# Kernel optimization log

Hardware: AMD Instinct MI355X
Metric: run time of the kernel (lower is better)

The kernel has to match this reference:

```python
import jax, jax.numpy as jnp
import numpy as np

CROSSOVER_MAGNITUDE = 0.3
MUTATION_FACTOR = 0.3

B, A, H = 16, 512, 8  # batch, activation_size (== dim_emb), n_head


def setup_inputs() -> dict:
    key = jax.random.key(0)
    ks = jax.random.split(key, 11)
    d = A
    s = 0.02  # small init scale for weights
    return {
        "Q": jax.random.normal(ks[0], (B, A, A), jnp.float32),
        "K": jax.random.normal(ks[1], (B, A, A), jnp.float32),
        "V": jax.random.normal(ks[2], (B, A), jnp.float32),
        "WQ_w": jax.random.normal(ks[3], (d, d), jnp.float32) * s,
        "WQ_b": jax.random.normal(ks[4], (d,), jnp.float32) * s,
        "WK_w": jax.random.normal(ks[5], (d, d), jnp.float32) * s,
        "WK_b": jax.random.normal(ks[6], (d,), jnp.float32) * s,
        "WV_w": jax.random.normal(ks[7], (d, d), jnp.float32) * s,
        "WV_b": jax.random.normal(ks[8], (d,), jnp.float32) * s,
        "WO_w": jax.random.normal(ks[9], (d, d * H), jnp.float32) * s,
        "WO_b": jax.random.normal(ks[10], (d,), jnp.float32) * s,
    }


def _attention_core(Qp, Kp, Vp, WO_w, WO_b):
    # Qp, Kp: (B, A, A) projected; identical across heads in the original
    # (heads are copies stacked before shared Linear), so compute once
    # and broadcast. Vp: (B, A).
    rkey = jax.random.key(42)
    kp, km, kr1, kr2 = jax.random.split(rkey, 4)

    am0 = jnp.einsum('bji,bjk->bik', Qp, Kp) / jnp.sqrt(jnp.float32(8.0))
    am = jnp.broadcast_to(am0[:, None], (B, H, A, A))  # (B,H,A,A)

    def mutate(a):
        # elementwise multiply by U(1-mf, 1+mf) noise
        m = jax.random.uniform(km, a.shape, jnp.float32,
                               1.0 - MUTATION_FACTOR, 1.0 + MUTATION_FACTOR)
        return a * m

    def crossover(a):
        # swap the tail segments [c:] of two random rows per (batch, head)
        c = A - int(A * CROSSOVER_MAGNITUDE)
        r1 = jax.random.randint(kr1, (B, H), 0, A)
        r2 = jax.random.randint(kr2, (B, H), 0, A)
        bi = jnp.arange(B)[:, None]
        hi = jnp.arange(H)[None, :]
        tails = a[..., c:]                     # (B,H,A,A-c)
        t1 = tails[bi, hi, r1]                 # (B,H,A-c)
        t2 = tails[bi, hi, r2]
        tails = tails.at[bi, hi, r1].set(t2).at[bi, hi, r2].set(t1)
        return jnp.concatenate([a[..., :c], tails], axis=-1)

    p = jax.random.uniform(kp, ())
    am = jax.lax.cond(p <= 0.6, mutate, crossover, am)

    attn = jax.nn.softmax(am, axis=-1)               # (B,H,A,A)
    out = jnp.einsum('bhij,bj->bhi', attn, Vp)       # attn @ V[...,None] squeezed
    out = out.reshape(B, H * A)
    return out @ WO_w.T + WO_b                       # (B, A)


def reference(Q, K, V, WQ_w, WQ_b, WK_w, WK_b, WV_w, WV_b, WO_w, WO_b):
    Qp = Q @ WQ_w.T + WQ_b   # (B,A,A), same for every head
    Kp = K @ WK_w.T + WK_b
    Vp = V @ WV_w.T + WV_b   # (B,A)
    return _attention_core(Qp, Kp, Vp, WO_w, WO_b)
```

## Files before the change

### kernel.cpp

```cpp
#include <hip/hip_runtime.h>
#include <stdint.h>
#include <string.h>

#define B_ 16
#define A_ 512
#define H_ 8
#define C_CROSS 359
#define LDSTRIDE 40

typedef short short8 __attribute__((ext_vector_type(8)));
typedef float floatx4 __attribute__((ext_vector_type(4)));

__host__ __device__ __forceinline__ uint32_t rotl32(uint32_t x, int r) {
#ifdef __HIP_DEVICE_COMPILE__
  return __builtin_amdgcn_alignbit(x, x, 32 - r);
#else
  return (x << r) | (x >> (32 - r));
#endif
}

__host__ __device__ __forceinline__ void tf2x32(uint32_t k0, uint32_t k1,
                                                uint32_t x0, uint32_t x1,
                                                uint32_t& o0, uint32_t& o1) {
  uint32_t ks2 = k0 ^ k1 ^ 0x1BD11BDAu;
  x0 += k0; x1 += k1;
#define TFR(r) { x0 += x1; x1 = rotl32(x1, r); x1 ^= x0; }
  TFR(13) TFR(15) TFR(26) TFR(6)   x0 += k1;  x1 += ks2 + 1u;
  TFR(17) TFR(29) TFR(16) TFR(24)  x0 += ks2; x1 += k0 + 2u;
  TFR(13) TFR(15) TFR(26) TFR(6)   x0 += k0;  x1 += k1 + 3u;
  TFR(17) TFR(29) TFR(16) TFR(24)  x0 += k1;  x1 += ks2 + 4u;
  TFR(13) TFR(15) TFR(26) TFR(6)   x0 += ks2; x1 += k0 + 5u;
#undef TFR
  o0 = x0; o1 = x1;
}

__host__ __device__ __forceinline__ float bits2u01(uint32_t bits) {
  uint32_t v = (bits >> 9) | 0x3f800000u;
  float f;
#ifdef __HIP_DEVICE_COMPILE__
  f = __uint_as_float(v);
#else
  memcpy(&f, &v, 4);
#endif
  return f - 1.0f;
}

__device__ __forceinline__ float exp2_native(float x) {
  float r;
  asm("v_exp_f32 %0, %1\n\ts_nop 0" : "=v"(r) : "v"(x));
  return r;
}

__device__ __forceinline__ void tsplit(float x, short& h, short& l) {
  uint32_t u = __float_as_uint(x);
  float hf = __uint_as_float(u & 0xffff0000u);
  h = (short)(u >> 16);
  l = (short)(__float_as_uint(x - hf) >> 16);
}

__device__ __forceinline__ void tsplit8(const float4& v0, const float4& v1,
                                        short8& h, short8& l) {
  float xs[8] = {v0.x, v0.y, v0.z, v0.w, v1.x, v1.y, v1.z, v1.w};
#pragma unroll
  for (int j = 0; j < 8; ++j) {
    short hh, ll;
    tsplit(xs[j], hh, ll);
    h[j] = hh; l[j] = ll;
  }
}

__global__ __launch_bounds__(256, 2) void lin_mfma2(
    const float* __restrict__ Xq, const float* __restrict__ Wq,
    const float* __restrict__ bq, ushort* __restrict__ QptH, ushort* __restrict__ QptL,
    const float* __restrict__ Xk, const float* __restrict__ Wk,
    const float* __restrict__ bk, ushort* __restrict__ KptH, ushort* __restrict__ KptL) {
  int bid = blockIdx.x;
  int z = bid >> 8;
  int rem = bid & 255;
  int ti = rem >> 2, tn = rem & 3;
  const float* X = z ? Xk : Xq;
  const float* W = z ? Wk : Wq;
  const float* bias = z ? bk : bq;
  ushort* OH = z ? KptH : QptH;
  ushort* OL = z ? KptL : QptL;

  __shared__ __align__(16) char smem[40960];
  ushort (*Ah)[LDSTRIDE] = (ushort(*)[LDSTRIDE])(smem);
  ushort (*Al)[LDSTRIDE] = (ushort(*)[LDSTRIDE])(smem + 10240);
  ushort (*Bh)[LDSTRIDE] = (ushort(*)[LDSTRIDE])(smem + 20480);
  ushort (*Bl)[LDSTRIDE] = (ushort(*)[LDSTRIDE])(smem + 30720);
  uint32_t (*cs)[132] = (uint32_t(*)[132])(smem);

  int tid = threadIdx.x;
  int w = tid >> 6, lane = tid & 63, quad = lane >> 4, l16 = lane & 15;
  int wm = (w >> 1) * 64, wn = (w & 1) * 64;
  int m0 = ti * 128;
  int n0 = tn * 128;

  float bv[4];
#pragma unroll
  for (int nt = 0; nt < 4; ++nt) bv[nt] = bias[n0 + wn + nt * 16 + l16];

  const float* pX[2];
  const float* pW[2];
  int mW[2], kgW[2];
#pragma unroll
  for (int g = 0; g < 2; ++g) {
    int gid = g * 256 + tid;
    int m = gid >> 2, kg = gid & 3;
    mW[g] = m; kgW[g] = kg;
    pX[g] = X + (size_t)(m0 + m) * 512 + kg * 8;
    pW[g] = W + (size_t)(n0 + m) * 512 + kg * 8;
  }

  float4 ra[2][2], rb[2][2];
#pragma unroll
  for (int g = 0; g < 2; ++g) {
    ra[g][0] = *(const float4*)(pX[g]);
    ra[g][1] = *(const float4*)(pX[g] + 4);
    rb[g][0] = *(const float4*)(pW[g]);
    rb[g][1] = *(const float4*)(pW[g] + 4);
  }

  floatx4 acc[4][4] = {};

  for (int k0 = 0; k0 < 512; k0 += 32) {
    __syncthreads();
#pragma unroll
    for (int g = 0; g < 2; ++g) {
      short8 h8, l8;
      tsplit8(ra[g][0], ra[g][1], h8, l8);
      *(short8*)&Ah[mW[g]][kgW[g] * 8] = h8;
      *(short8*)&Al[mW[g]][kgW[g] * 8] = l8;
      tsplit8(rb[g][0], rb[g][1], h8, l8);
      *(short8*)&Bh[mW[g]][kgW[g] * 8] = h8;
      *(short8*)&Bl[mW[g]][kgW[g] * 8] = l8;
    }
    __syncthreads();
    if (k0 < 480) {
      int kn = k0 + 32;
#pragma unroll
      for (int g = 0; g < 2; ++g) {
        ra[g][0] = *(const float4*)(pX[g] + kn);
        ra[g][1] = *(const float4*)(pX[g] + kn + 4);
        rb[g][0] = *(const float4*)(pW[g] + kn);
        rb[g][1] = *(const float4*)(pW[g] + kn + 4);
      }
    }
    short8 fAh[4], fAl[4], fBh[4], fBl[4];
#pragma unroll
    for (int t4 = 0; t4 < 4; ++t4) {
      int ma = wm + t4 * 16 + l16;
      int nb = wn + t4 * 16 + l16;
      fAh[t4] = *(const short8*)&Ah[ma][quad * 8];
      fAl[t4] = *(const short8*)&Al[ma][quad * 8];
      fBh[t4] = *(const short8*)&Bh[nb][quad * 8];
      fBl[t4] = *(const short8*)&Bl[nb][quad * 8];
    }
#pragma unroll
    for (int mt = 0; mt < 4; ++mt)
#pragma unroll
      for (int nt = 0; nt < 4; ++nt) {
        acc[mt][nt] = __builtin_amdgcn_mfma_f32_16x16x32_bf16(fAh[mt], fBh[nt], acc[mt][nt], 0, 0, 0);
        acc[mt][nt] = __builtin_amdgcn_mfma_f32_16x16x32_bf16(fAh[mt], fBl[nt], acc[mt][nt], 0, 0, 0);
        acc[mt][nt] = __builtin_amdgcn_mfma_f32_16x16x32_bf16(fAl[mt], fBh[nt], acc[mt][nt], 0, 0, 0);
      }
  }

  __syncthreads();
  int bb = m0 >> 9, i0 = m0 & 511;
  for (int p = 0; p < 2; ++p) {
    if ((w & 1) == p) {
#pragma unroll
      for (int mt = 0; mt < 4; ++mt)
#pragma unroll
        for (int nt = 0; nt < 4; ++nt)
#pragma unroll
          for (int rr = 0; rr < 4; ++rr) {
            float val = acc[mt][nt][rr] + bv[nt];
            uint32_t u = __float_as_uint(val);
            uint32_t hi = u & 0xffff0000u;
            uint32_t lo = __float_as_uint(val - __uint_as_float(hi)) >> 16;
            cs[nt * 16 + l16][wm + mt * 16 + quad * 4 + rr] = hi | lo;
          }
    }
    __syncthreads();
    {
      int col_l = tid >> 2, iseg = (tid & 3) * 32;
      int d = n0 + p * 64 + col_l;
      size_t obase = ((size_t)(bb * 512 + d)) * 512 + i0 + iseg;
      ushort* oh = OH + obase;
      ushort* ol = OL + obase;
#pragma unroll
      for (int sgi = 0; sgi < 4; ++sgi) {
        short8 hv, lv;
#pragma unroll
        for (int j = 0; j < 8; ++j) {
          uint32_t v = cs[col_l][iseg + sgi * 8 + j];
          hv[j] = (short)(v >> 16);
          lv[j] = (short)(v & 0xffffu);
        }
        *(short8*)(oh + sgi * 8) = hv;
        *(short8*)(ol + sgi * 8) = lv;
      }
    }
    __syncthreads();
  }
}

__global__ __launch_bounds__(256, 2) void am_mfma2(
    const ushort* __restrict__ QH, const ushort* __restrict__ QL,
    const ushort* __restrict__ KH, const ushort* __restrict__ KL,
    float* __restrict__ am0) {
  int bid = blockIdx.x;
  int xcd = bid & 7, slot = bid >> 3;
  int bz = xcd + 8 * (slot >> 4);
  int tt = slot & 15, ti = tt >> 2, tk = tt & 3;
  int bm0 = ti * 128, bn0 = tk * 128;
  size_t base = (size_t)bz * 262144;

  __shared__ __align__(16) char smem[40960];
  ushort (*Ah)[LDSTRIDE] = (ushort(*)[LDSTRIDE])(smem);
  ushort (*Al)[LDSTRIDE] = (ushort(*)[LDSTRIDE])(smem + 10240);
  ushort (*Bh)[LDSTRIDE] = (ushort(*)[LDSTRIDE])(smem + 20480);
  ushort (*Bl)[LDSTRIDE] = (ushort(*)[LDSTRIDE])(smem + 30720);

  int tid = threadIdx.x;
  int w = tid >> 6, lane = tid & 63, quad = lane >> 4, l16 = lane & 15;
  int wm = (w >> 1) * 64, wn = (w & 1) * 64;

  const ushort *pAH[2], *pAL[2], *pBH[2], *pBL[2];
  int mW[2], kgW[2];
#pragma unroll
  for (int g = 0; g < 2; ++g) {
    int gid = g * 256 + tid;
    int m = gid >> 2, kg = gid & 3;
    mW[g] = m; kgW[g] = kg;
    size_t offA = base + (size_t)(bm0 + m) * 512 + kg * 8;
    size_t offB = base + (size_t)(bn0 + m) * 512 + kg * 8;
    pAH[g] = QH + offA; pAL[g] = QL + offA;
    pBH[g] = KH + offB; pBL[g] = KL + offB;
  }

  short8 rah[2], ral[2], rbh[2], rbl[2];
#pragma unroll
  for (int g = 0; g < 2; ++g) {
    rah[g] = *(const short8*)(pAH[g]);
    ral[g] = *(const short8*)(pAL[g]);
    rbh[g] = *(const short8*)(pBH[g]);
    rbl[g] = *(const short8*)(pBL[g]);
  }

  floatx4 acc[4][4] = {};

  for (int k0 = 0; k0 < 512; k0 += 32) {
    __syncthreads();
#pragma unroll
    for (int g = 0; g < 2; ++g) {
      *(short8*)&Ah[mW[g]][kgW[g] * 8] = rah[g];
      *(short8*)&Al[mW[g]][kgW[g] * 8] = ral[g];
      *(short8*)&Bh[mW[g]][kgW[g] * 8] = rbh[g];
      *(short8*)&Bl[mW[g]][kgW[g] * 8] = rbl[g];
    }
    __syncthreads();
    if (k0 < 480) {
      int kn = k0 + 32;
#pragma unroll
      for (int g = 0; g < 2; ++g) {
        rah[g] = *(const short8*)(pAH[g] + kn);
        ral[g] = *(const short8*)(pAL[g] + kn);
        rbh[g] = *(const short8*)(pBH[g] + kn);
        rbl[g] = *(const short8*)(pBL[g] + kn);
      }
    }
    short8 fAh[4], fAl[4], fBh[4], fBl[4];
#pragma unroll
    for (int t4 = 0; t4 < 4; ++t4) {
      int ma = wm + t4 * 16 + l16;
      int nb = wn + t4 * 16 + l16;
      fAh[t4] = *(const short8*)&Ah[ma][quad * 8];
      fAl[t4] = *(const short8*)&Al[ma][quad * 8];
      fBh[t4] = *(const short8*)&Bh[nb][quad * 8];
      fBl[t4] = *(const short8*)&Bl[nb][quad * 8];
    }
#pragma unroll
    for (int mt = 0; mt < 4; ++mt)
#pragma unroll
      for (int nt = 0; nt < 4; ++nt) {
        acc[mt][nt] = __builtin_amdgcn_mfma_f32_16x16x32_bf16(fAh[mt], fBh[nt], acc[mt][nt], 0, 0, 0);
        acc[mt][nt] = __builtin_amdgcn_mfma_f32_16x16x32_bf16(fAh[mt], fBl[nt], acc[mt][nt], 0, 0, 0);
        acc[mt][nt] = __builtin_amdgcn_mfma_f32_16x16x32_bf16(fAl[mt], fBh[nt], acc[mt][nt], 0, 0, 0);
      }
  }
  const float scale = 0.35355339059327373f;
#pragma unroll
  for (int mt = 0; mt < 4; ++mt)
#pragma unroll
    for (int nt = 0; nt < 4; ++nt)
#pragma unroll
      for (int rr = 0; rr < 4; ++rr) {
        int row = bm0 + wm + mt * 16 + quad * 4 + rr;
        int col = bn0 + wn + nt * 16 + l16;
        am0[((size_t)(bz * 512 + row)) * 512 + col] = acc[mt][nt][rr] * scale;
      }
}

__global__ __launch_bounds__(256) void small_gemm(
    const float* __restrict__ X, const float* __restrict__ W,
    const float* __restrict__ bias, float* __restrict__ out, int K) {
  __shared__ float xs[16 * 260];
  __shared__ float ws[16 * 260];
  int tid = threadIdx.x;
  int j0 = blockIdx.x * 16;
  int k0 = blockIdx.y * 256;
#pragma unroll
  for (int it = 0; it < 4; ++it) {
    int idx = it * 256 + tid;
    int rr = idx >> 6, kk4 = idx & 63;
    float4 xv = *(const float4*)(X + (size_t)rr * K + k0 + kk4 * 4);
    float4 wv = *(const float4*)(W + (size_t)(j0 + rr) * K + k0 + kk4 * 4);
    *(float4*)&xs[rr * 260 + kk4 * 4] = xv;
    *(float4*)&ws[rr * 260 + kk4 * 4] = wv;
  }
  __syncthreads();
  int b = tid & 15, j = tid >> 4;
  const float* xr = &xs[b * 260];
  const float* wr = &ws[j * 260];
  float acc = 0.f;
#pragma unroll
  for (int kk = 0; kk < 256; kk += 4) {
    float4 a = *(const float4*)(xr + kk);
    float4 w4 = *(const float4*)(wr + kk);
    acc += a.x * w4.x + a.y * w4.y + a.z * w4.z + a.w * w4.w;
  }
  if (blockIdx.y == 0) acc += bias[j0 + j];
  atomicAdd(&out[b * 512 + j0 + j], acc);
}

__global__ __launch_bounds__(256) void soft_mut(
    const float* __restrict__ am0, const float* __restrict__ Vp,
    float* __restrict__ oa, uint32_t km0, uint32_t km1) {
  int tid = threadIdx.x;
  int w = tid >> 6, lane = tid & 63;
  int rrow = blockIdx.x * 4 + w;
  int b = rrow >> 9, i = rrow & 511;
  int k0 = lane * 8;
  const float* ar = am0 + (((size_t)rrow) << 9) + k0;
  const float* vr = Vp + (b << 9) + k0;
  float4 a0 = *(const float4*)ar, a1 = *(const float4*)(ar + 4);
  float4 v0 = *(const float4*)vr, v1 = *(const float4*)(vr + 4);
  const float LOG2E = 1.4426950408889634f;
  float a2[8] = {a0.x * LOG2E, a0.y * LOG2E, a0.z * LOG2E, a0.w * LOG2E,
                 a1.x * LOG2E, a1.y * LOG2E, a1.z * LOG2E, a1.w * LOG2E};
  float vv[8] = {v0.x, v0.y, v0.z, v0.w, v1.x, v1.y, v1.z, v1.w};
  uint32_t Lbase = (uint32_t)b * 2097152u + (uint32_t)i * 512u + (uint32_t)k0;
  float outv[8];
#pragma unroll
  for (int h = 0; h < 8; ++h) {
    uint32_t Lh = Lbase + (uint32_t)h * 262144u;
    float s = 0.f, wsum = 0.f;
#pragma unroll
    for (int j = 0; j < 8; ++j) {
      uint32_t o0, o1;
      tf2x32(km0, km1, 0u, Lh + (uint32_t)j, o0, o1);
      uint32_t bits = o0 ^ o1;
      float f = __uint_as_float((bits >> 9) | 0x3f800000u);
      float m = fmaxf(0.7f, __builtin_fmaf(f, 0.6f, 0.1f));
      float e = exp2_native(a2[j] * m);
      s += e;
      wsum += e * vv[j];
    }
#pragma unroll
    for (int o = 32; o; o >>= 1) { s += __shfl_xor(s, o); wsum += __shfl_xor(wsum, o); }
    outv[h] = wsum / s;
  }
  if (lane == 0) {
    int ob = (b << 12) + i;
#pragma unroll
    for (int h = 0; h < 8; ++h) oa[ob + (h << 9)] = outv[h];
  }
}

struct CrossCfg { int r1[B_ * H_]; int r2[B_ * H_]; };

__global__ __launch_bounds__(256) void soft_cross(
    const float* __restrict__ am0, const float* __restrict__ Vp,
    float* __restrict__ oa, CrossCfg cfg) {
  int tid = threadIdx.x;
  int w = tid >> 6, lane = tid & 63;
  int rrow = blockIdx.x * 4 + w;
  int b = rrow >> 12, h = (rrow >> 9) & 7, i = rrow & 511;
  int rr1 = cfg.r1[b * 8 + h], rr2 = cfg.r2[b * 8 + h];
  int src = (i == rr2) ? rr1 : ((i == rr1) ? rr2 : i);
  const float* ar = am0 + ((size_t)((b << 9) + i)) * A_;
  const float* ar2 = am0 + ((size_t)((b << 9) + src)) * A_;
  const float* vr = Vp + (b << 9);
  float s = 0.f, wsum = 0.f;
#pragma unroll
  for (int j = 0; j < 8; ++j) {
    int k = lane + 64 * j;
    float x = (k >= C_CROSS) ? ar2[k] : ar[k];
    float e = __expf(x);
    s += e;
    wsum += e * vr[k];
  }
#pragma unroll
  for (int o = 32; o; o >>= 1) { s += __shfl_xor(s, o); wsum += __shfl_xor(wsum, o); }
  if (lane == 0) oa[(((size_t)(b * 8 + h)) << 9) + i] = wsum / s;
}

extern "C" void kernel_launch(void* const* d_in, const int* in_sizes, int n_in,
                              void* d_out, int out_size, void* d_ws, size_t ws_size,
                              hipStream_t stream) {
  (void)in_sizes; (void)n_in; (void)out_size; (void)ws_size;
  const float* Q    = (const float*)d_in[0];
  const float* K    = (const float*)d_in[1];
  const float* V    = (const float*)d_in[2];
  const float* WQ_w = (const float*)d_in[3];
  const float* WQ_b = (const float*)d_in[4];
  const float* WK_w = (const float*)d_in[5];
  const float* WK_b = (const float*)d_in[6];
  const float* WV_w = (const float*)d_in[7];
  const float* WV_b = (const float*)d_in[8];
  const float* WO_w = (const float*)d_in[9];
  const float* WO_b = (const float*)d_in[10];
  float* out = (float*)d_out;

  char* ws = (char*)d_ws;
  ushort* QptH = (ushort*)(ws);
  ushort* QptL = (ushort*)(ws + (size_t)8388608);
  ushort* KptH = (ushort*)(ws + (size_t)16777216);
  ushort* KptL = (ushort*)(ws + (size_t)25165824);
  float*  am0  = (float*) (ws + (size_t)33554432);
  float*  Vp   = (float*) (ws + (size_t)50331648);
  float*  oa   = (float*) (ws + (size_t)50331648 + 65536);

  uint32_t kp0, kp1, km0, km1, kr10, kr11, kr20, kr21, a, bbits;
  tf2x32(0u, 42u, 0u, 0u, kp0, kp1);
  tf2x32(0u, 42u, 0u, 1u, km0, km1);
  tf2x32(0u, 42u, 0u, 2u, kr10, kr11);
  tf2x32(0u, 42u, 0u, 3u, kr20, kr21);
  tf2x32(kp0, kp1, 0u, 0u, a, bbits);
  float p = bits2u01(a ^ bbits);
  if (p < 0.f) p = 0.f;
  bool mutate = (p <= 0.6f);

  hipMemsetAsync(Vp, 0, 16 * 512 * sizeof(float), stream);
  hipMemsetAsync(out, 0, 16 * 512 * sizeof(float), stream);

  lin_mfma2<<<512, 256, 0, stream>>>(Q, WQ_w, WQ_b, QptH, QptL,
                                     K, WK_w, WK_b, KptH, KptL);
  small_gemm<<<dim3(32, 2), 256, 0, stream>>>(V, WV_w, WV_b, Vp, 512);
  am_mfma2<<<256, 256, 0, stream>>>(QptH, QptL, KptH, KptL, am0);
  if (mutate) {
    soft_mut<<<2048, 256, 0, stream>>>(am0, Vp, oa, km0, km1);
  } else {
    CrossCfg cfg;
    uint32_t c0, c1;
    tf2x32(kr10, kr11, 0u, 1u, c0, c1);
    for (int t = 0; t < B_ * H_; ++t) {
      tf2x32(c0, c1, 0u, (uint32_t)t, a, bbits);
      cfg.r1[t] = (int)((a ^ bbits) & 511u);
    }
    tf2x32(kr20, kr21, 0u, 1u, c0, c1);
    for (int t = 0; t < B_ * H_; ++t) {
      tf2x32(c0, c1, 0u, (uint32_t)t, a, bbits);
      cfg.r2[t] = (int)((a ^ bbits) & 511u);
    }
    soft_cross<<<16384, 256, 0, stream>>>(am0, Vp, oa, cfg);
  }
  small_gemm<<<dim3(32, 16), 256, 0, stream>>>(oa, WO_w, WO_b, out, 4096);
}
```

Before: 222.7 us.

## Precompute mutation noise in spare GEMM blocks and pre-split weights to bf16 pairs

Adds extra blocks to the projection and attention-matrix GEMM launches that generate the Threefry mutation noise into a workspace buffer, so the softmax kernel only reads precomputed bits instead of running the RNG inline. It also adds a kernel that splits WQ/WK into bf16 high/low halves once, so the projection GEMM loads pre-split weights rather than converting them every tile. The new path depends on workspace size and adds 16M×2 bytes of noise traffic plus an extra launch, in exchange for overlapping RNG work with MFMA-bound kernels.

```diff
diff --git a/kernel.cpp b/kernel.cpp
--- a/kernel.cpp
+++ b/kernel.cpp
@@ -9,6 +9,7 @@
 #define LDSTRIDE 40
 
 typedef short short8 __attribute__((ext_vector_type(8)));
+typedef unsigned short us8 __attribute__((ext_vector_type(8)));
 typedef float floatx4 __attribute__((ext_vector_type(4)));
 
 __host__ __device__ __forceinline__ uint32_t rotl32(uint32_t x, int r) {
@@ -66,6 +67,191 @@
     short hh, ll;
     tsplit(xs[j], hh, ll);
     h[j] = hh; l[j] = ll;
+  }
+}
+
+__device__ __forceinline__ void genmul_chunk(ushort* __restrict__ mbits, int chunk,
+                                             uint32_t km0, uint32_t km1) {
+  int t = threadIdx.x;
+  uint32_t base = (uint32_t)chunk * 16384u;
+#pragma unroll
+  for (int j = 0; j < 8; ++j) {
+    uint32_t L0 = base + (uint32_t)j * 2048u + (uint32_t)t * 8u;
+    us8 out;
+#pragma unroll
+    for (int q = 0; q < 8; ++q) {
+      uint32_t o0, o1;
+      tf2x32(km0, km1, 0u, L0 + (uint32_t)q, o0, o1);
+      out[q] = (unsigned short)((o0 ^ o1) >> 16);
+    }
+    *(us8*)(mbits + L0) = out;
+  }
+}
+
+__global__ __launch_bounds__(256) void presplitW(
+    const float* __restrict__ Wq, ushort* __restrict__ WqH, ushort* __restrict__ WqL,
+    const float* __restrict__ Wk, ushort* __restrict__ WkH, ushort* __restrict__ WkL) {
+  int gid = blockIdx.x * 256 + threadIdx.x;
+  int z = gid >> 15;
+  size_t e0 = (size_t)(gid & 32767) * 8;
+  const float* W = z ? Wk : Wq;
+  ushort* WH = z ? WkH : WqH;
+  ushort* WL = z ? WkL : WqL;
+  float4 v0 = *(const float4*)(W + e0);
+  float4 v1 = *(const float4*)(W + e0 + 4);
+  short8 h8, l8;
+  tsplit8(v0, v1, h8, l8);
+  *(short8*)(WH + e0) = h8;
+  *(short8*)(WL + e0) = l8;
+}
+
+__global__ __launch_bounds__(256, 2) void lin3(
+    const float* __restrict__ Xq,
+    const ushort* __restrict__ WqH, const ushort* __restrict__ WqL,
+    const float* __restrict__ bq, ushort* __restrict__ QptH, ushort* __restrict__ QptL,
+    const float* __restrict__ Xk,
+    const ushort* __restrict__ WkH, const ushort* __restrict__ WkL,
+    const float* __restrict__ bk, ushort* __restrict__ KptH, ushort* __restrict__ KptL,
+    ushort* __restrict__ mbits, int genOff, uint32_t km0, uint32_t km1) {
+  int bid = blockIdx.x;
+  if (bid >= 512) {
+    genmul_chunk(mbits, genOff + (bid - 512), km0, km1);
+    return;
+  }
+  int z = bid >> 8;
+  int rem = bid & 255;
+  int ti = rem >> 2, tn = rem & 3;
+  const float* X = z ? Xk : Xq;
+  const ushort* WH = z ? WkH : WqH;
+  const ushort* WL = z ? WkL : WqL;
+  const float* bias = z ? bk : bq;
+  ushort* OH = z ? KptH : QptH;
+  ushort* OL = z ? KptL : QptL;
+
+  __shared__ __align__(16) char smem[40960];
+  ushort (*Ah)[LDSTRIDE] = (ushort(*)[LDSTRIDE])(smem);
+  ushort (*Al)[LDSTRIDE] = (ushort(*)[LDSTRIDE])(smem + 10240);
+  ushort (*Bh)[LDSTRIDE] = (ushort(*)[LDSTRIDE])(smem + 20480);
+  ushort (*Bl)[LDSTRIDE] = (ushort(*)[LDSTRIDE])(smem + 30720);
+  uint32_t (*cs)[132] = (uint32_t(*)[132])(smem);
+
+  int tid = threadIdx.x;
+  int w = tid >> 6, lane = tid & 63, quad = lane >> 4, l16 = lane & 15;
+  int wm = (w >> 1) * 64, wn = (w & 1) * 64;
+  int m0 = ti * 128;
+  int n0 = tn * 128;
+
+  float bv[4];
+#pragma unroll
+  for (int nt = 0; nt < 4; ++nt) bv[nt] = bias[n0 + wn + nt * 16 + l16];
+
+  const float* pX[2];
+  const ushort* pWH[2];
+  const ushort* pWL[2];
+  int mW[2], kgW[2];
+#pragma unroll
+  for (int g = 0; g < 2; ++g) {
+    int gid = g * 256 + tid;
+    int m = gid >> 2, kg = gid & 3;
+    mW[g] = m; kgW[g] = kg;
+    pX[g] = X + (size_t)(m0 + m) * 512 + kg * 8;
+    size_t woff = (size_t)(n0 + m) * 512 + kg * 8;
+    pWH[g] = WH + woff;
+    pWL[g] = WL + woff;
+  }
+
+  float4 ra[2][2];
+  short8 rbh[2], rbl[2];
+#pragma unroll
+  for (int g = 0; g < 2; ++g) {
+    ra[g][0] = *(const float4*)(pX[g]);
+    ra[g][1] = *(const float4*)(pX[g] + 4);
+    rbh[g] = *(const short8*)(pWH[g]);
+    rbl[g] = *(const short8*)(pWL[g]);
+  }
+
+  floatx4 acc[4][4] = {};
+
+  for (int k0 = 0; k0 < 512; k0 += 32) {
+    __syncthreads();
+#pragma unroll
+    for (int g = 0; g < 2; ++g) {
+      short8 h8, l8;
+      tsplit8(ra[g][0], ra[g][1], h8, l8);
+      *(short8*)&Ah[mW[g]][kgW[g] * 8] = h8;
+      *(short8*)&Al[mW[g]][kgW[g] * 8] = l8;
+      *(short8*)&Bh[mW[g]][kgW[g] * 8] = rbh[g];
+      *(short8*)&Bl[mW[g]][kgW[g] * 8] = rbl[g];
+    }
+    __syncthreads();
+    if (k0 < 480) {
+      int kn = k0 + 32;
+#pragma unroll
+      for (int g = 0; g < 2; ++g) {
+        ra[g][0] = *(const float4*)(pX[g] + kn);
+        ra[g][1] = *(const float4*)(pX[g] + kn + 4);
+        rbh[g] = *(const short8*)(pWH[g] + kn);
+        rbl[g] = *(const short8*)(pWL[g] + kn);
+      }
+    }
+    short8 fAh[4], fAl[4], fBh[4], fBl[4];
+#pragma unroll
+    for (int t4 = 0; t4 < 4; ++t4) {
+      int ma = wm + t4 * 16 + l16;
+      int nb = wn + t4 * 16 + l16;
+      fAh[t4] = *(const short8*)&Ah[ma][quad * 8];
+      fAl[t4] = *(const short8*)&Al[ma][quad * 8];
+      fBh[t4] = *(const short8*)&Bh[nb][quad * 8];
+      fBl[t4] = *(const short8*)&Bl[nb][quad * 8];
+    }
+#pragma unroll
+    for (int mt = 0; mt < 4; ++mt)
+#pragma unroll
+      for (int nt = 0; nt < 4; ++nt) {
+        acc[mt][nt] = __builtin_amdgcn_mfma_f32_16x16x32_bf16(fAh[mt], fBh[nt], acc[mt][nt], 0, 0, 0);
+        acc[mt][nt] = __builtin_amdgcn_mfma_f32_16x16x32_bf16(fAh[mt], fBl[nt], acc[mt][nt], 0, 0, 0);
+        acc[mt][nt] = __builtin_amdgcn_mfma_f32_16x16x32_bf16(fAl[mt], fBh[nt], acc[mt][nt], 0, 0, 0);
+      }
+  }
+
+  __syncthreads();
+  int bb = m0 >> 9, i0 = m0 & 511;
+  for (int p = 0; p < 2; ++p) {
+    if ((w & 1) == p) {
+#pragma unroll
+      for (int mt = 0; mt < 4; ++mt)
+#pragma unroll
+        for (int nt = 0; nt < 4; ++nt)
+#pragma unroll
+          for (int rr = 0; rr < 4; ++rr) {
+            float val = acc[mt][nt][rr] + bv[nt];
+            uint32_t u = __float_as_uint(val);
+            uint32_t hi = u & 0xffff0000u;
+            uint32_t lo = __float_as_uint(val - __uint_as_float(hi)) >> 16;
+            cs[nt * 16 + l16][wm + mt * 16 + quad * 4 + rr] = hi | lo;
+          }
+    }
+    __syncthreads();
+    {
+      int col_l = tid >> 2, iseg = (tid & 3) * 32;
+      int d = n0 + p * 64 + col_l;
+      size_t obase = ((size_t)(bb * 512 + d)) * 512 + i0 + iseg;
+      ushort* oh = OH + obase;
+      ushort* ol = OL + obase;
+#pragma unroll
+      for (int sgi = 0; sgi < 4; ++sgi) {
+        short8 hv, lv;
+#pragma unroll
+        for (int j = 0; j < 8; ++j) {
+          uint32_t v = cs[col_l][iseg + sgi * 8 + j];
+          hv[j] = (short)(v >> 16);
+          lv[j] = (short)(v & 0xffffu);
+        }
+        *(short8*)(oh + sgi * 8) = hv;
+        *(short8*)(ol + sgi * 8) = lv;
+      }
+    }
+    __syncthreads();
   }
 }
 
@@ -208,11 +394,16 @@
   }
 }
 
-__global__ __launch_bounds__(256, 2) void am_mfma2(
+__global__ __launch_bounds__(256, 2) void am3(
     const ushort* __restrict__ QH, const ushort* __restrict__ QL,
     const ushort* __restrict__ KH, const ushort* __restrict__ KL,
-    float* __restrict__ am0) {
+    float* __restrict__ am0,
+    ushort* __restrict__ mbits, int genOff, uint32_t km0, uint32_t km1) {
   int bid = blockIdx.x;
+  if (bid >= 256) {
+    genmul_chunk(mbits, genOff + (bid - 256), km0, km1);
+    return;
+  }
   int xcd = bid & 7, slot = bid >> 3;
   int bz = xcd + 8 * (slot >> 4);
   int tt = slot & 15, ti = tt >> 2, tk = tt & 3;
@@ -335,6 +526,47 @@
   }
   if (blockIdx.y == 0) acc += bias[j0 + j];
   atomicAdd(&out[b * 512 + j0 + j], acc);
+}
+
+__global__ __launch_bounds__(256) void soft_mut_pre(
+    const float* __restrict__ am0, const float* __restrict__ Vp,
+    const ushort* __restrict__ mbits, float* __restrict__ oa) {
+  int tid = threadIdx.x;
+  int w = tid >> 6, lane = tid & 63;
+  int rrow = blockIdx.x * 4 + w;
+  int b = rrow >> 9, i = rrow & 511;
+  int k0 = lane * 8;
+  const float* ar = am0 + (((size_t)rrow) << 9) + k0;
+  const float* vr = Vp + (b << 9) + k0;
+  float4 a0 = *(const float4*)ar, a1 = *(const float4*)(ar + 4);
+  float4 v0 = *(const float4*)vr, v1 = *(const float4*)(vr + 4);
+  const float LOG2E = 1.4426950408889634f;
+  float a2[8] = {a0.x * LOG2E, a0.y * LOG2E, a0.z * LOG2E, a0.w * LOG2E,
+                 a1.x * LOG2E, a1.y * LOG2E, a1.z * LOG2E, a1.w * LOG2E};
+  float vv[8] = {v0.x, v0.y, v0.z, v0.w, v1.x, v1.y, v1.z, v1.w};
+  float outv[8];
+#pragma unroll
+  for (int h = 0; h < 8; ++h) {
+    us8 mb = *(const us8*)(mbits + ((((size_t)(b * 8 + h)) << 18) + ((size_t)i << 9) + k0));
+    float s = 0.f, wsum = 0.f;
+#pragma unroll
+    for (int j = 0; j < 8; ++j) {
+      uint32_t fb = (((uint32_t)mb[j]) << 7) | 0x3f800000u;
+      float f = __uint_as_float(fb);
+      float m = fmaxf(0.7f, __builtin_fmaf(f, 0.6f, 0.1f));
+      float e = exp2_native(a2[j] * m);
+      s += e;
+      wsum += e * vv[j];
+    }
+#pragma unroll
+    for (int o = 32; o; o >>= 1) { s += __shfl_xor(s, o); wsum += __shfl_xor(wsum, o); }
+    outv[h] = wsum / s;
+  }
+  if (lane == 0) {
+    int ob = (b << 12) + i;
+#pragma unroll
+    for (int h = 0; h < 8; ++h) oa[ob + (h << 9)] = outv[h];
+  }
 }
 
 __global__ __launch_bounds__(256) void soft_mut(
@@ -412,7 +644,7 @@
 extern "C" void kernel_launch(void* const* d_in, const int* in_sizes, int n_in,
                               void* d_out, int out_size, void* d_ws, size_t ws_size,
                               hipStream_t stream) {
-  (void)in_sizes; (void)n_in; (void)out_size; (void)ws_size;
+  (void)in_sizes; (void)n_in; (void)out_size;
   const float* Q    = (const float*)d_in[0];
   const float* K    = (const float*)d_in[1];
   const float* V    = (const float*)d_in[2];
@@ -433,7 +665,15 @@
   ushort* KptL = (ushort*)(ws + (size_t)25165824);
   float*  am0  = (float*) (ws + (size_t)33554432);
   float*  Vp   = (float*) (ws + (size_t)50331648);
-  float*  oa   = (float*) (ws + (size_t)50331648 + 65536);
+  float*  oa   = (float*) (ws + (size_t)50397184);
+  ushort* WqH  = (ushort*)(ws + (size_t)50659328);
+  ushort* WqL  = (ushort*)(ws + (size_t)51183616);
+  ushort* WkH  = (ushort*)(ws + (size_t)51707904);
+  ushort* WkL  = (ushort*)(ws + (size_t)52232192);
+  ushort* mbits= (ushort*)(ws + (size_t)52756480);
+
+  int tier = (ws_size >= (size_t)119865344) ? 0
+           : (ws_size >= (size_t)52756480) ? 1 : 2;
 
   uint32_t kp0, kp1, km0, km1, kr10, kr11, kr20, kr21, a, bbits;
   tf2x32(0u, 42u, 0u, 0u, kp0, kp1);
@@ -448,12 +688,27 @@
   hipMemsetAsync(Vp, 0, 16 * 512 * sizeof(float), stream);
   hipMemsetAsync(out, 0, 16 * 512 * sizeof(float), stream);
 
-  lin_mfma2<<<512, 256, 0, stream>>>(Q, WQ_w, WQ_b, QptH, QptL,
-                                     K, WK_w, WK_b, KptH, KptL);
+  if (tier <= 1) {
+    presplitW<<<256, 256, 0, stream>>>(WQ_w, WqH, WqL, WK_w, WkH, WkL);
+    int linGrid = (tier == 0 && mutate) ? 512 + 1024 : 512;
+    lin3<<<linGrid, 256, 0, stream>>>(Q, WqH, WqL, WQ_b, QptH, QptL,
+                                      K, WkH, WkL, WK_b, KptH, KptL,
+                                      mbits, 0, km0, km1);
+  } else {
+    lin_mfma2<<<512, 256, 0, stream>>>(Q, WQ_w, WQ_b, QptH, QptL,
+                                       K, WK_w, WK_b, KptH, KptL);
+  }
   small_gemm<<<dim3(32, 2), 256, 0, stream>>>(V, WV_w, WV_b, Vp, 512);
-  am_mfma2<<<256, 256, 0, stream>>>(QptH, QptL, KptH, KptL, am0);
+  {
+    int amGrid = (tier == 0 && mutate) ? 256 + 1024 : 256;
+    am3<<<amGrid, 256, 0, stream>>>(QptH, QptL, KptH, KptL, am0,
+                                    mbits, 1024, km0, km1);
+  }
   if (mutate) {
-    soft_mut<<<2048, 256, 0, stream>>>(am0, Vp, oa, km0, km1);
+    if (tier == 0)
+      soft_mut_pre<<<2048, 256, 0, stream>>>(am0, Vp, mbits, oa);
+    else
+      soft_mut<<<2048, 256, 0, stream>>>(am0, Vp, oa, km0, km1);
   } else {
     CrossCfg cfg;
     uint32_t c0, c1;
```

New measurement: 222.2 us. About the same (-0.3%).

## Pre-split projection weights and overlap mutation RNG generation with GEMM kernels

Applied to the files above, without the earlier changes.

Adds a kernel that splits WQ/WK into bf16 hi/lo once and also computes Vp, so the projection GEMM loads pre-split weights instead of re-splitting them per tile. When the workspace is large enough and the mutate branch is taken, the Threefry mutation bits are generated inside the two MFMA GEMM kernels and stored as 16-bit values. A new softmax kernel then reads those bits instead of running the RNG itself. This hides RNG ALU work under the memory- and MFMA-bound GEMMs, at the cost of extra global traffic for the mbits buffer and a workspace-size-dependent code path.

```diff
diff --git a/kernel.cpp b/kernel.cpp
--- a/kernel.cpp
+++ b/kernel.cpp
@@ -9,6 +9,7 @@
 #define LDSTRIDE 40
 
 typedef short short8 __attribute__((ext_vector_type(8)));
+typedef unsigned short us8 __attribute__((ext_vector_type(8)));
 typedef float floatx4 __attribute__((ext_vector_type(4)));
 
 __host__ __device__ __forceinline__ uint32_t rotl32(uint32_t x, int r) {
@@ -51,35 +52,94 @@
   return r;
 }
 
-__device__ __forceinline__ void tsplit(float x, short& h, short& l) {
-  uint32_t u = __float_as_uint(x);
-  float hf = __uint_as_float(u & 0xffff0000u);
-  h = (short)(u >> 16);
-  l = (short)(__float_as_uint(x - hf) >> 16);
-}
-
 __device__ __forceinline__ void tsplit8(const float4& v0, const float4& v1,
                                         short8& h, short8& l) {
   float xs[8] = {v0.x, v0.y, v0.z, v0.w, v1.x, v1.y, v1.z, v1.w};
 #pragma unroll
   for (int j = 0; j < 8; ++j) {
-    short hh, ll;
-    tsplit(xs[j], hh, ll);
-    h[j] = hh; l[j] = ll;
-  }
-}
-
-__global__ __launch_bounds__(256, 2) void lin_mfma2(
-    const float* __restrict__ Xq, const float* __restrict__ Wq,
+    uint32_t u = __float_as_uint(xs[j]);
+    float hf = __uint_as_float(u & 0xffff0000u);
+    h[j] = (short)(u >> 16);
+    l[j] = (short)(__float_as_uint(xs[j] - hf) >> 16);
+  }
+}
+
+__device__ __forceinline__ void gen8(ushort* mbits, uint32_t L0,
+                                     uint32_t km0, uint32_t km1) {
+  us8 o;
+#pragma unroll
+  for (int q = 0; q < 8; ++q) {
+    uint32_t a, b;
+    tf2x32(km0, km1, 0u, L0 + (uint32_t)q, a, b);
+    o[q] = (unsigned short)((a ^ b) >> 16);
+  }
+  *(us8*)(mbits + L0) = o;
+}
+
+__global__ __launch_bounds__(256) void presplit_vp(
+    const float* __restrict__ Wq, ushort* __restrict__ WqH, ushort* __restrict__ WqL,
+    const float* __restrict__ Wk, ushort* __restrict__ WkH, ushort* __restrict__ WkL,
+    const float* __restrict__ V, const float* __restrict__ WV_w,
+    const float* __restrict__ WV_b, float* __restrict__ Vp) {
+  int bid = blockIdx.x, tid = threadIdx.x;
+  if (bid < 256) {
+    int gid = bid * 256 + tid;
+    int z = gid >> 15;
+    size_t e0 = (size_t)(gid & 32767) * 8;
+    const float* W = z ? Wk : Wq;
+    ushort* WH = z ? WkH : WqH;
+    ushort* WL = z ? WkL : WqL;
+    float4 v0 = *(const float4*)(W + e0);
+    float4 v1 = *(const float4*)(W + e0 + 4);
+    short8 h8, l8;
+    tsplit8(v0, v1, h8, l8);
+    *(short8*)(WH + e0) = h8;
+    *(short8*)(WL + e0) = l8;
+    return;
+  }
+  __shared__ float xs[16 * 260];
+  __shared__ float wsh[16 * 260];
+  int v = bid - 256;
+  int j0 = (v >> 1) * 16, k0 = (v & 1) * 256;
+#pragma unroll
+  for (int it = 0; it < 4; ++it) {
+    int idx = it * 256 + tid;
+    int rr = idx >> 6, kk4 = idx & 63;
+    float4 xv = *(const float4*)(V + (size_t)rr * 512 + k0 + kk4 * 4);
+    float4 wv = *(const float4*)(WV_w + (size_t)(j0 + rr) * 512 + k0 + kk4 * 4);
+    *(float4*)&xs[rr * 260 + kk4 * 4] = xv;
+    *(float4*)&wsh[rr * 260 + kk4 * 4] = wv;
+  }
+  __syncthreads();
+  int b = tid & 15, j = tid >> 4;
+  const float* xr = &xs[b * 260];
+  const float* wr = &wsh[j * 260];
+  float acc = 0.f;
+#pragma unroll
+  for (int kk = 0; kk < 256; kk += 4) {
+    float4 a = *(const float4*)(xr + kk);
+    float4 w4 = *(const float4*)(wr + kk);
+    acc += a.x * w4.x + a.y * w4.y + a.z * w4.z + a.w * w4.w;
+  }
+  if ((v & 1) == 0) acc += WV_b[j0 + j];
+  atomicAdd(&Vp[b * 512 + j0 + j], acc);
+}
+
+__global__ __launch_bounds__(256, 2) void lin3h(
+    const float* __restrict__ Xq,
+    const ushort* __restrict__ WqH, const ushort* __restrict__ WqL,
     const float* __restrict__ bq, ushort* __restrict__ QptH, ushort* __restrict__ QptL,
-    const float* __restrict__ Xk, const float* __restrict__ Wk,
-    const float* __restrict__ bk, ushort* __restrict__ KptH, ushort* __restrict__ KptL) {
+    const float* __restrict__ Xk,
+    const ushort* __restrict__ WkH, const ushort* __restrict__ WkL,
+    const float* __restrict__ bk, ushort* __restrict__ KptH, ushort* __restrict__ KptL,
+    ushort* __restrict__ mbits, int doGen, uint32_t km0, uint32_t km1) {
   int bid = blockIdx.x;
   int z = bid >> 8;
   int rem = bid & 255;
   int ti = rem >> 2, tn = rem & 3;
   const float* X = z ? Xk : Xq;
-  const float* W = z ? Wk : Wq;
+  const ushort* WH = z ? WkH : WqH;
+  const ushort* WL = z ? WkL : WqL;
   const float* bias = z ? bk : bq;
   ushort* OH = z ? KptH : QptH;
   ushort* OL = z ? KptL : QptL;
@@ -94,15 +154,15 @@
   int tid = threadIdx.x;
   int w = tid >> 6, lane = tid & 63, quad = lane >> 4, l16 = lane & 15;
   int wm = (w >> 1) * 64, wn = (w & 1) * 64;
-  int m0 = ti * 128;
-  int n0 = tn * 128;
+  int m0 = ti * 128, n0 = tn * 128;
 
   float bv[4];
 #pragma unroll
   for (int nt = 0; nt < 4; ++nt) bv[nt] = bias[n0 + wn + nt * 16 + l16];
 
   const float* pX[2];
-  const float* pW[2];
+  const ushort* pWH[2];
+  const ushort* pWL[2];
   int mW[2], kgW[2];
 #pragma unroll
   for (int g = 0; g < 2; ++g) {
@@ -110,18 +170,22 @@
     int m = gid >> 2, kg = gid & 3;
     mW[g] = m; kgW[g] = kg;
     pX[g] = X + (size_t)(m0 + m) * 512 + kg * 8;
-    pW[g] = W + (size_t)(n0 + m) * 512 + kg * 8;
-  }
-
-  float4 ra[2][2], rb[2][2];
+    size_t woff = (size_t)(n0 + m) * 512 + kg * 8;
+    pWH[g] = WH + woff;
+    pWL[g] = WL + woff;
+  }
+
+  float4 ra[2][2];
+  short8 rbh[2], rbl[2];
 #pragma unroll
   for (int g = 0; g < 2; ++g) {
     ra[g][0] = *(const float4*)(pX[g]);
     ra[g][1] = *(const float4*)(pX[g] + 4);
-    rb[g][0] = *(const float4*)(pW[g]);
-    rb[g][1] = *(const float4*)(pW[g] + 4);
-  }
-
+    rbh[g] = *(const short8*)(pWH[g]);
+    rbl[g] = *(const short8*)(pWL[g]);
+  }
+
+  uint32_t genBase = (uint32_t)bid * 32768u + (uint32_t)tid * 8u;
   floatx4 acc[4][4] = {};
 
   for (int k0 = 0; k0 < 512; k0 += 32) {
@@ -132,9 +196,8 @@
       tsplit8(ra[g][0], ra[g][1], h8, l8);
       *(short8*)&Ah[mW[g]][kgW[g] * 8] = h8;
       *(short8*)&Al[mW[g]][kgW[g] * 8] = l8;
-      tsplit8(rb[g][0], rb[g][1], h8, l8);
-      *(short8*)&Bh[mW[g]][kgW[g] * 8] = h8;
-      *(short8*)&Bl[mW[g]][kgW[g] * 8] = l8;
+      *(short8*)&Bh[mW[g]][kgW[g] * 8] = rbh[g];
+      *(short8*)&Bl[mW[g]][kgW[g] * 8] = rbl[g];
     }
     __syncthreads();
     if (k0 < 480) {
@@ -143,10 +206,12 @@
       for (int g = 0; g < 2; ++g) {
         ra[g][0] = *(const float4*)(pX[g] + kn);
         ra[g][1] = *(const float4*)(pX[g] + kn + 4);
-        rb[g][0] = *(const float4*)(pW[g] + kn);
-        rb[g][1] = *(const float4*)(pW[g] + kn + 4);
+        rbh[g] = *(const short8*)(pWH[g] + kn);
+        rbl[g] = *(const short8*)(pWL[g] + kn);
       }
     }
+    if (doGen) gen8(mbits, genBase + (uint32_t)(k0 >> 5) * 2048u, km0, km1);
+
     short8 fAh[4], fAl[4], fBh[4], fBl[4];
 #pragma unroll
     for (int t4 = 0; t4 < 4; ++t4) {
@@ -208,10 +273,11 @@
   }
 }
 
-__global__ __launch_bounds__(256, 2) void am_mfma2(
+__global__ __launch_bounds__(256, 2) void am3h(
     const ushort* __restrict__ QH, const ushort* __restrict__ QL,
     const ushort* __restrict__ KH, const ushort* __restrict__ KL,
-    float* __restrict__ am0) {
+    float* __restrict__ am0,
+    ushort* __restrict__ mbits, int doGen, uint32_t km0, uint32_t km1) {
   int bid = blockIdx.x;
   int xcd = bid & 7, slot = bid >> 3;
   int bz = xcd + 8 * (slot >> 4);
@@ -251,6 +317,7 @@
     rbl[g] = *(const short8*)(pBL[g]);
   }
 
+  uint32_t genBase = 16777216u + (uint32_t)bid * 65536u + (uint32_t)tid * 8u;
   floatx4 acc[4][4] = {};
 
   for (int k0 = 0; k0 < 512; k0 += 32) {
@@ -272,6 +339,11 @@
         rbh[g] = *(const short8*)(pBH[g] + kn);
         rbl[g] = *(const short8*)(pBL[g] + kn);
       }
+    }
+    if (doGen) {
+      uint32_t gb = genBase + (uint32_t)(k0 >> 5) * 4096u;
+      gen8(mbits, gb, km0, km1);
+      gen8(mbits, gb + 2048u, km0, km1);
     }
     short8 fAh[4], fAl[4], fBh[4], fBl[4];
 #pragma unroll
@@ -335,6 +407,47 @@
   }
   if (blockIdx.y == 0) acc += bias[j0 + j];
   atomicAdd(&out[b * 512 + j0 + j], acc);
+}
+
+__global__ __launch_bounds__(256) void soft_mut_pre(
+    const float* __restrict__ am0, const float* __restrict__ Vp,
+    const ushort* __restrict__ mbits, float* __restrict__ oa) {
+  int tid = threadIdx.x;
+  int w = tid >> 6, lane = tid & 63;
+  int rrow = blockIdx.x * 4 + w;
+  int b = rrow >> 9, i = rrow & 511;
+  int k0 = lane * 8;
+  const float* ar = am0 + (((size_t)rrow) << 9) + k0;
+  const float* vr = Vp + (b << 9) + k0;
+  float4 a0 = *(const float4*)ar, a1 = *(const float4*)(ar + 4);
+  float4 v0 = *(const float4*)vr, v1 = *(const float4*)(vr + 4);
+  const float LOG2E = 1.4426950408889634f;
+  float a2[8] = {a0.x * LOG2E, a0.y * LOG2E, a0.z * LOG2E, a0.w * LOG2E,
+                 a1.x * LOG2E, a1.y * LOG2E, a1.z * LOG2E, a1.w * LOG2E};
+  float vv[8] = {v0.x, v0.y, v0.z, v0.w, v1.x, v1.y, v1.z, v1.w};
+  float outv[8];
+#pragma unroll
+  for (int h = 0; h < 8; ++h) {
+    us8 mb = *(const us8*)(mbits + ((((size_t)(b * 8 + h)) << 18) + ((size_t)i << 9) + k0));
+    float s = 0.f, wsum = 0.f;
+#pragma unroll
+    for (int j = 0; j < 8; ++j) {
+      uint32_t fb = (((uint32_t)mb[j]) << 7) | 0x3f800000u;
+      float f = __uint_as_float(fb);
+      float m = fmaxf(0.7f, __builtin_fmaf(f, 0.6f, 0.1f));
+      float e = exp2_native(a2[j] * m);
+      s += e;
+      wsum += e * vv[j];
+    }
+#pragma unroll
+    for (int o = 32; o; o >>= 1) { s += __shfl_xor(s, o); wsum += __shfl_xor(wsum, o); }
+    outv[h] = wsum / s;
+  }
+  if (lane == 0) {
+    int ob = (b << 12) + i;
+#pragma unroll
+    for (int h = 0; h < 8; ++h) oa[ob + (h << 9)] = outv[h];
+  }
 }
 
 __global__ __launch_bounds__(256) void soft_mut(
@@ -412,7 +525,7 @@
 extern "C" void kernel_launch(void* const* d_in, const int* in_sizes, int n_in,
                               void* d_out, int out_size, void* d_ws, size_t ws_size,
                               hipStream_t stream) {
-  (void)in_sizes; (void)n_in; (void)out_size; (void)ws_size;
+  (void)in_sizes; (void)n_in; (void)out_size;
   const float* Q    = (const float*)d_in[0];
   const float* K    = (const float*)d_in[1];
   const float* V    = (const float*)d_in[2];
@@ -433,7 +546,15 @@
   ushort* KptL = (ushort*)(ws + (size_t)25165824);
   float*  am0  = (float*) (ws + (size_t)33554432);
   float*  Vp   = (float*) (ws + (size_t)50331648);
-  float*  oa   = (float*) (ws + (size_t)50331648 + 65536);
+  float*  oa   = (float*) (ws + (size_t)50364416);
+  ushort* WqH  = (ushort*)(ws + (size_t)50659328);
+  ushort* WqL  = (ushort*)(ws + (size_t)51183616);
+  ushort* WkH  = (ushort*)(ws + (size_t)51707904);
+  ushort* WkL  = (ushort*)(ws + (size_t)52232192);
+  ushort* mbits= (ushort*)(ws + (size_t)52756480);
+
+  int tier = (ws_size >= (size_t)119865344) ? 0
+           : (ws_size >= (size_t)52756480) ? 1 : 2;
 
   uint32_t kp0, kp1, km0, km1, kr10, kr11, kr20, kr21, a, bbits;
   tf2x32(0u, 42u, 0u, 0u, kp0, kp1);
@@ -444,16 +565,35 @@
   float p = bits2u01(a ^ bbits);
   if (p < 0.f) p = 0.f;
   bool mutate = (p <= 0.6f);
-
-  hipMemsetAsync(Vp, 0, 16 * 512 * sizeof(float), stream);
+  int doGen = (mutate && tier == 0) ? 1 : 0;
+
+  hipMemsetAsync(Vp, 0, 32768, stream);
   hipMemsetAsync(out, 0, 16 * 512 * sizeof(float), stream);
 
-  lin_mfma2<<<512, 256, 0, stream>>>(Q, WQ_w, WQ_b, QptH, QptL,
-                                     K, WK_w, WK_b, KptH, KptL);
-  small_gemm<<<dim3(32, 2), 256, 0, stream>>>(V, WV_w, WV_b, Vp, 512);
-  am_mfma2<<<256, 256, 0, stream>>>(QptH, QptL, KptH, KptL, am0);
+  if (tier <= 1) {
+    presplit_vp<<<320, 256, 0, stream>>>(WQ_w, WqH, WqL, WK_w, WkH, WkL,
+                                         V, WV_w, WV_b, Vp);
+    lin3h<<<512, 256, 0, stream>>>(Q, WqH, WqL, WQ_b, QptH, QptL,
+                                   K, WkH, WkL, WK_b, KptH, KptL,
+                                   mbits, doGen, km0, km1);
+  } else {
+    ushort* tWqH = (ushort*)(ws + (size_t)33554432);
+    ushort* tWqL = tWqH + 262144;
+    ushort* tWkH = tWqL + 262144;
+    ushort* tWkL = tWkH + 262144;
+    presplit_vp<<<320, 256, 0, stream>>>(WQ_w, tWqH, tWqL, WK_w, tWkH, tWkL,
+                                         V, WV_w, WV_b, Vp);
+    lin3h<<<512, 256, 0, stream>>>(Q, tWqH, tWqL, WQ_b, QptH, QptL,
+                                   K, tWkH, tWkL, WK_b, KptH, KptL,
+                                   mbits, 0, km0, km1);
+  }
+  am3h<<<256, 256, 0, stream>>>(QptH, QptL, KptH, KptL, am0,
+                                mbits, doGen, km0, km1);
   if (mutate) {
-    soft_mut<<<2048, 256, 0, stream>>>(am0, Vp, oa, km0, km1);
+    if (doGen)
+      soft_mut_pre<<<2048, 256, 0, stream>>>(am0, Vp, mbits, oa);
+    else
+      soft_mut<<<2048, 256, 0, stream>>>(am0, Vp, oa, km0, km1);
   } else {
     CrossCfg cfg;
     uint32_t c0, c1;
```

Measured after the change: 238.3 us. +7.0%, slower.
